# Optimization experiments

Hardware: AMD Instinct MI355X
Metric: run time of the kernel (lower is better)

Reference implementation:

```python
import jax, jax.numpy as jnp
import numpy as np


def _temperature_scales():
    s = np.arange(8, -3, -0.25).astype(np.float32)  # 44 levels
    s[-1] = 0.0
    return jnp.asarray(s)


def _pdist2(x, y):
    # squared euclidean distance matrix: [B,N,M]
    x_norm = jnp.sum(x * x, axis=2, keepdims=True)          # [B,N,1]
    y_norm = jnp.sum(y * y, axis=2, keepdims=True)          # [B,M,1]
    cross = jnp.einsum('bnd,bmd->bnm', x, y)
    return x_norm - 2.0 * cross + jnp.swapaxes(y_norm, 1, 2)


def _compute_match(points_x, points_y):
    b, n, _ = points_x.shape
    _, m, _ = points_y.shape
    max_size = max(n, m)
    factorl = max_size / n
    factorr = max_size / m
    d2 = _pdist2(points_x, points_y)                        # [B,N,M]
    satl0 = jnp.full((b, n), factorl, dtype=points_x.dtype)
    satr0 = jnp.full((b, m), factorr, dtype=points_x.dtype)
    match0 = jnp.zeros_like(d2)

    def step(carry, level):
        satl, satr, match = carry
        log_sr = jnp.log(satr[:, None, :] + 1e-30)          # [B,1,M]
        weight = jax.nn.softmax(d2 * level + log_sr, axis=-1)
        weight = weight * satl[:, :, None]
        ss = jnp.sum(weight, axis=1, keepdims=True) + 1e-09  # [B,1,M]
        ss = jnp.minimum(satr[:, None, :] / ss, 1.0)
        weight = weight * ss
        s = jnp.sum(weight, axis=2)                          # [B,N]
        ss2 = jnp.sum(weight, axis=1)                        # [B,M]
        satl = jnp.maximum(satl - s, 0.0)
        satr = jnp.maximum(satr - ss2, 0.0)
        match = match + weight
        return (satl, satr, match), None

    (_, _, match), _ = jax.lax.scan(step, (satl0, satr0, match0), _temperature_scales())
    return jax.lax.stop_gradient(match)


def setup_inputs() -> dict:
    key = jax.random.key(0)
    kx, ky = jax.random.split(key)
    B, N, M, D = 16, 2048, 2048, 3
    return {
        'points_x': jax.random.normal(kx, (B, N, D), dtype=jnp.float32),
        'points_y': jax.random.normal(ky, (B, M, D), dtype=jnp.float32),
    }


def reference(points_x, points_y):
    match = _compute_match(points_x, points_y)               # [B,N,M], detached
    d2 = _pdist2(points_x, points_y)                         # [B,N,M]
    loss = jnp.mean(jnp.sum(match * d2, axis=(1, 2)))
    return loss
```

## Files before the change

### kernel.cpp

```cpp
#include <hip/hip_runtime.h>

constexpr int NB = 16, NN = 2048, NM = 2048;
constexpr float LOG2E = 1.4426950408889634f;

#define EXP2 __builtin_amdgcn_exp2f
#define LOG2 __builtin_amdgcn_logf

constexpr size_t W_SATL  = 0;
constexpr size_t W_SATR  = 32768;
constexpr size_t W_ROWA  = 65536;
constexpr size_t W_ROWB  = 65536 + 4*32768;
constexpr size_t W_SPART = W_ROWB + 4*32768;
constexpr size_t W_LOSS  = W_SPART + (size_t)NB*32*NN;

__global__ __launch_bounds__(256) void k_init(float* ws) {
  int i = blockIdx.x*256 + threadIdx.x;
  if (i < NB*NM) ws[W_SATR + i] = 1.0f;
  if (i == 0) ws[W_LOSS] = 0.0f;
}

__global__ __launch_bounds__(512) void k_rows(const float* __restrict__ px,
                                              const float* __restrict__ py,
                                              float* __restrict__ ws,
                                              float lvl2, int first) {
  __shared__ float4 cpk[NM];
  const int b  = blockIdx.x >> 5;
  const int rb = blockIdx.x & 31;
  const int tid = threadIdx.x;

  {
    const float* satr = ws + W_SATR + (size_t)b*NM;
    const float4* pyv = (const float4*)(py + (size_t)b*NM*3);
    float4 pA = pyv[tid*3+0], pB = pyv[tid*3+1], pC = pyv[tid*3+2];
    float yy[12] = {pA.x,pA.y,pA.z,pA.w, pB.x,pB.y,pB.z,pB.w, pC.x,pC.y,pC.z,pC.w};
    #pragma unroll
    for (int k = 0; k < 4; ++k) {
      int col = tid*4 + k;
      float y0 = yy[3*k], y1 = yy[3*k+1], y2 = yy[3*k+2];
      float yn = y0*y0 + y1*y1 + y2*y2;
      float c  = fmaf(yn, lvl2, LOG2(satr[col] + 1e-30f));
      cpk[col] = make_float4(y0, y1, y2, c);
    }
  }
  __syncthreads();

  const int rloc = tid >> 3;
  const int q    = tid & 7;
  const int row  = rb*64 + rloc;
  const size_t gn = (size_t)b*NN + row;
  float x0 = px[gn*3+0], x1 = px[gn*3+1], x2 = px[gn*3+2];
  float xn = x0*x0 + x1*x1 + x2*x2;
  float an = xn * lvl2;
  float scl = -2.0f * lvl2;
  float xs0 = scl*x0, xs1 = scl*x1, xs2 = scl*x2;

  float rmax = -3.402823466e38f, rsum = 0.0f;
  for (int c8 = 0; c8 < 32; ++c8) {
    float l[8];
    #pragma unroll
    for (int i = 0; i < 8; ++i) {
      int col = (c8*8 + i)*8 + q;
      float4 p = cpk[col];
      l[i] = fmaf(xs0, p.x, fmaf(xs1, p.y, fmaf(xs2, p.z, p.w + an)));
    }
    float m01 = fmaxf(l[0], l[1]), m23 = fmaxf(l[2], l[3]);
    float m45 = fmaxf(l[4], l[5]), m67 = fmaxf(l[6], l[7]);
    float cm  = fmaxf(fmaxf(m01, m23), fmaxf(m45, m67));
    float nm  = fmaxf(rmax, cm);
    float cs = 0.0f;
    #pragma unroll
    for (int i = 0; i < 8; ++i) cs += EXP2(l[i] - nm);
    rsum = fmaf(rsum, EXP2(rmax - nm), cs);
    rmax = nm;
  }

  float sp = 0.0f;
  if (!first) {
    const float* spart = ws + W_SPART + ((size_t)b*32)*NN;
    #pragma unroll
    for (int i = 0; i < 4; ++i) sp += spart[(size_t)(q*4 + i)*NN + row];
  }

  #pragma unroll
  for (int d = 1; d <= 4; d <<= 1) {
    float om  = __shfl_xor(rmax, d);
    float od  = __shfl_xor(rsum, d);
    float osp = __shfl_xor(sp,  d);
    float nm  = fmaxf(rmax, om);
    rsum = rsum*EXP2(rmax - nm) + od*EXP2(om - nm);
    rmax = nm;
    sp += osp;
  }

  if (q == 0) {
    float sl = first ? 1.0f : ws[W_SATL + gn];
    sl = fmaxf(sl - sp, 0.0f);
    ws[W_SATL + gn] = sl;
    float rs2 = LOG2(sl / rsum) - rmax;
    float4* rowA = (float4*)(ws + W_ROWA);
    float4* rowB = (float4*)(ws + W_ROWB);
    rowA[gn] = make_float4(xs0, xs1, xs2, rs2 + an);
    rowB[gn] = make_float4(x0, x1, x2, rs2);
  }
}

__global__ __launch_bounds__(512) void k_cols(const float* __restrict__ py,
                                              float* __restrict__ ws,
                                              float lvl2) {
  __shared__ float4 rowLDS[NN];
  __shared__ float  sspart[8][64];
  __shared__ float4 colLDS[64];
  __shared__ float  lred[8];
  const int tid = threadIdx.x;
  const int wv = tid >> 6, lane = tid & 63;
  const int b = blockIdx.x >> 5, tile = blockIdx.x & 31;
  const int col = tile*64 + lane;
  const size_t gm = (size_t)b*NM + col;

  float y0 = py[gm*3+0], y1 = py[gm*3+1], y2 = py[gm*3+2];
  float yn = y0*y0 + y1*y1 + y2*y2;
  float sr  = ws[W_SATR + gm];
  float lsr = LOG2(sr + 1e-30f);
  float cB  = fmaf(yn, lvl2, lsr);

  const float4* gRowA = (const float4*)(ws + W_ROWA) + (size_t)b*NN;
  for (int i = tid; i < NN; i += 512) rowLDS[i] = gRowA[i];
  __syncthreads();

  const int n0 = wv * 256;
  float acc = 0.0f;
  #pragma unroll 8
  for (int n = n0; n < n0 + 256; ++n) {
    float4 r = rowLDS[n];
    float t = fmaf(r.x, y0, fmaf(r.y, y1, fmaf(r.z, y2, r.w + cB)));
    acc += EXP2(t);
  }
  sspart[wv][lane] = acc;
  __syncthreads();
  if (wv == 0) {
    float S = 0.0f;
    #pragma unroll
    for (int w = 0; w < 8; ++w) S += sspart[w][lane];
    float ssc = fminf(sr / (S + 1e-9f), 1.0f);
    float cC  = lsr + LOG2(ssc);
    ws[W_SATR + gm] = fmaxf(sr - S*ssc, 0.0f);
    colLDS[lane] = make_float4(y0, y1, y2, cC);
  }
  __syncthreads();

  const float4* gRowB = (const float4*)(ws + W_ROWB) + (size_t)b*NN;
  float* spart = ws + W_SPART + ((size_t)b*32 + tile)*NN;
  float4 r0 = gRowB[0*512 + tid];
  float4 r1 = gRowB[1*512 + tid];
  float4 r2 = gRowB[2*512 + tid];
  float4 r3 = gRowB[3*512 + tid];
  float s0 = 0.f, s1 = 0.f, s2 = 0.f, s3 = 0.f;
  float lossa = 0.0f;
  #pragma unroll 4
  for (int c = 0; c < 64; ++c) {
    float4 cv = colLDS[c];
    {
      float d0 = r0.x-cv.x, d1 = r0.y-cv.y, dz = r0.z-cv.z;
      float d2 = fmaf(d0,d0, fmaf(d1,d1, dz*dz));
      float w  = EXP2(fmaf(d2, lvl2, r0.w + cv.w));
      lossa = fmaf(w, d2, lossa); s0 += w;
    }
    {
      float d0 = r1.x-cv.x, d1 = r1.y-cv.y, dz = r1.z-cv.z;
      float d2 = fmaf(d0,d0, fmaf(d1,d1, dz*dz));
      float w  = EXP2(fmaf(d2, lvl2, r1.w + cv.w));
      lossa = fmaf(w, d2, lossa); s1 += w;
    }
    {
      float d0 = r2.x-cv.x, d1 = r2.y-cv.y, dz = r2.z-cv.z;
      float d2 = fmaf(d0,d0, fmaf(d1,d1, dz*dz));
      float w  = EXP2(fmaf(d2, lvl2, r2.w + cv.w));
      lossa = fmaf(w, d2, lossa); s2 += w;
    }
    {
      float d0 = r3.x-cv.x, d1 = r3.y-cv.y, dz = r3.z-cv.z;
      float d2 = fmaf(d0,d0, fmaf(d1,d1, dz*dz));
      float w  = EXP2(fmaf(d2, lvl2, r3.w + cv.w));
      lossa = fmaf(w, d2, lossa); s3 += w;
    }
  }
  spart[0*512 + tid] = s0;
  spart[1*512 + tid] = s1;
  spart[2*512 + tid] = s2;
  spart[3*512 + tid] = s3;

  #pragma unroll
  for (int d = 32; d >= 1; d >>= 1) lossa += __shfl_xor(lossa, d);
  if (lane == 0) lred[wv] = lossa;
  __syncthreads();
  if (tid == 0) {
    float t = 0.f;
    #pragma unroll
    for (int w = 0; w < 8; ++w) t += lred[w];
    atomicAdd(ws + W_LOSS, t);
  }
}

__global__ void k_final(const float* __restrict__ ws, float* __restrict__ out) {
  out[0] = ws[W_LOSS] * (1.0f / (float)NB);
}

extern "C" void kernel_launch(void* const* d_in, const int* in_sizes, int n_in,
                              void* d_out, int out_size, void* d_ws, size_t ws_size,
                              hipStream_t stream) {
  const float* px = (const float*)d_in[0];
  const float* py = (const float*)d_in[1];
  float* ws  = (float*)d_ws;
  float* out = (float*)d_out;

  k_init<<<dim3((NB*NM + 255)/256), dim3(256), 0, stream>>>(ws);
  for (int lv = 0; lv < 44; ++lv) {
    float level = (lv == 43) ? 0.0f : (8.0f - 0.25f*(float)lv);
    float lvl2 = level * LOG2E;
    k_rows<<<dim3(NB*32), dim3(512), 0, stream>>>(px, py, ws, lvl2, lv == 0 ? 1 : 0);
    k_cols<<<dim3(NB*32), dim3(512), 0, stream>>>(py, ws, lvl2);
  }
  k_final<<<dim3(1), dim3(1), 0, stream>>>(ws, out);
}
```

Before: 2.542 ms.

## Interleave row/column pairs and use packed FP32 FMA math

Row and column data move from one float4 per point to a pair-interleaved layout (x of two points, y of two points, and so on), so the distance and logit arithmetic can run as two-wide packed FP32 FMA, max and add ops. This applies to the softmax pass in the row kernel and to both passes in the column kernel. The row-kernel writeback becomes scattered scalar stores to match the new layout. The aim is to cut VALU instruction count, while exp2 stays scalar, and the changed LDS and global access pattern may alter bank conflicts or store efficiency.

```diff
diff --git a/kernel.cpp b/kernel.cpp
--- a/kernel.cpp
+++ b/kernel.cpp
@@ -5,6 +5,16 @@
 
 #define EXP2 __builtin_amdgcn_exp2f
 #define LOG2 __builtin_amdgcn_logf
+
+typedef float f32x2 __attribute__((ext_vector_type(2)));
+typedef float f32x4 __attribute__((ext_vector_type(4)));
+
+static __device__ __forceinline__ f32x2 pk_fma(f32x2 a, f32x2 b, f32x2 c) {
+  return __builtin_elementwise_fma(a, b, c);
+}
+static __device__ __forceinline__ f32x2 pk_max(f32x2 a, f32x2 b) {
+  return __builtin_elementwise_max(a, b);
+}
 
 constexpr size_t W_SATL  = 0;
 constexpr size_t W_SATR  = 32768;
@@ -23,7 +33,7 @@
                                               const float* __restrict__ py,
                                               float* __restrict__ ws,
                                               float lvl2, int first) {
-  __shared__ float4 cpk[NM];
+  __shared__ f32x4 cpk[NM];
   const int b  = blockIdx.x >> 5;
   const int rb = blockIdx.x & 31;
   const int tid = threadIdx.x;
@@ -33,13 +43,21 @@
     const float4* pyv = (const float4*)(py + (size_t)b*NM*3);
     float4 pA = pyv[tid*3+0], pB = pyv[tid*3+1], pC = pyv[tid*3+2];
     float yy[12] = {pA.x,pA.y,pA.z,pA.w, pB.x,pB.y,pB.z,pB.w, pC.x,pC.y,pC.z,pC.w};
+    float cm[4];
     #pragma unroll
     for (int k = 0; k < 4; ++k) {
       int col = tid*4 + k;
       float y0 = yy[3*k], y1 = yy[3*k+1], y2 = yy[3*k+2];
       float yn = y0*y0 + y1*y1 + y2*y2;
-      float c  = fmaf(yn, lvl2, LOG2(satr[col] + 1e-30f));
-      cpk[col] = make_float4(y0, y1, y2, c);
+      cm[k] = fmaf(yn, lvl2, LOG2(satr[col] + 1e-30f));
+    }
+    #pragma unroll
+    for (int k2 = 0; k2 < 2; ++k2) {
+      int ka = 2*k2, kb = 2*k2+1;
+      f32x4 lo = {yy[3*ka], yy[3*kb], yy[3*ka+1], yy[3*kb+1]};
+      f32x4 hi = {yy[3*ka+2], yy[3*kb+2], cm[ka], cm[kb]};
+      cpk[(2*tid + k2)*2 + 0] = lo;
+      cpk[(2*tid + k2)*2 + 1] = hi;
     }
   }
   __syncthreads();
@@ -53,23 +71,25 @@
   float an = xn * lvl2;
   float scl = -2.0f * lvl2;
   float xs0 = scl*x0, xs1 = scl*x1, xs2 = scl*x2;
+  f32x2 xs0p = {xs0,xs0}, xs1p = {xs1,xs1}, xs2p = {xs2,xs2}, anp = {an,an};
 
   float rmax = -3.402823466e38f, rsum = 0.0f;
   for (int c8 = 0; c8 < 32; ++c8) {
-    float l[8];
-    #pragma unroll
-    for (int i = 0; i < 8; ++i) {
-      int col = (c8*8 + i)*8 + q;
-      float4 p = cpk[col];
-      l[i] = fmaf(xs0, p.x, fmaf(xs1, p.y, fmaf(xs2, p.z, p.w + an)));
-    }
-    float m01 = fmaxf(l[0], l[1]), m23 = fmaxf(l[2], l[3]);
-    float m45 = fmaxf(l[4], l[5]), m67 = fmaxf(l[6], l[7]);
-    float cm  = fmaxf(fmaxf(m01, m23), fmaxf(m45, m67));
+    f32x2 lp[4];
+    #pragma unroll
+    for (int i = 0; i < 4; ++i) {
+      int pj = (c8*4 + i)*8 + q;
+      f32x4 a  = cpk[2*pj];
+      f32x4 b2 = cpk[2*pj+1];
+      lp[i] = pk_fma(xs0p, a.xy, pk_fma(xs1p, a.zw, pk_fma(xs2p, b2.xy, b2.zw + anp)));
+    }
+    f32x2 mp = pk_max(pk_max(lp[0], lp[1]), pk_max(lp[2], lp[3]));
+    float cm  = fmaxf(mp.x, mp.y);
     float nm  = fmaxf(rmax, cm);
-    float cs = 0.0f;
-    #pragma unroll
-    for (int i = 0; i < 8; ++i) cs += EXP2(l[i] - nm);
+    f32x2 nms = {nm, nm};
+    f32x2 e0 = lp[0] - nms, e1 = lp[1] - nms, e2 = lp[2] - nms, e3 = lp[3] - nms;
+    float cs = ((EXP2(e0.x) + EXP2(e0.y)) + (EXP2(e1.x) + EXP2(e1.y)))
+             + ((EXP2(e2.x) + EXP2(e2.y)) + (EXP2(e3.x) + EXP2(e3.y)));
     rsum = fmaf(rsum, EXP2(rmax - nm), cs);
     rmax = nm;
   }
@@ -97,17 +117,18 @@
     sl = fmaxf(sl - sp, 0.0f);
     ws[W_SATL + gn] = sl;
     float rs2 = LOG2(sl / rsum) - rmax;
-    float4* rowA = (float4*)(ws + W_ROWA);
-    float4* rowB = (float4*)(ws + W_ROWB);
-    rowA[gn] = make_float4(xs0, xs1, xs2, rs2 + an);
-    rowB[gn] = make_float4(x0, x1, x2, rs2);
+    size_t pbase = (size_t)b*NN*4 + (size_t)(row >> 1)*8 + (row & 1);
+    float* A  = ws + W_ROWA + pbase;
+    float* Bq = ws + W_ROWB + pbase;
+    A[0] = xs0; A[2] = xs1; A[4] = xs2; A[6] = rs2 + an;
+    Bq[0] = x0; Bq[2] = x1; Bq[4] = x2; Bq[6] = rs2;
   }
 }
 
 __global__ __launch_bounds__(512) void k_cols(const float* __restrict__ py,
                                               float* __restrict__ ws,
                                               float lvl2) {
-  __shared__ float4 rowLDS[NN];
+  __shared__ f32x4 rowLDS[NN];
   __shared__ float  sspart[8][64];
   __shared__ float4 colLDS[64];
   __shared__ float  lred[8];
@@ -123,19 +144,22 @@
   float lsr = LOG2(sr + 1e-30f);
   float cB  = fmaf(yn, lvl2, lsr);
 
-  const float4* gRowA = (const float4*)(ws + W_ROWA) + (size_t)b*NN;
+  const f32x4* gRowA = (const f32x4*)(ws + W_ROWA) + (size_t)b*NN;
   for (int i = tid; i < NN; i += 512) rowLDS[i] = gRowA[i];
   __syncthreads();
 
-  const int n0 = wv * 256;
-  float acc = 0.0f;
+  const int p0 = wv * 128;
+  f32x2 y0p = {y0,y0}, y1p = {y1,y1}, y2p = {y2,y2}, cBp = {cB,cB};
+  f32x2 accp = {0.f, 0.f};
   #pragma unroll 8
-  for (int n = n0; n < n0 + 256; ++n) {
-    float4 r = rowLDS[n];
-    float t = fmaf(r.x, y0, fmaf(r.y, y1, fmaf(r.z, y2, r.w + cB)));
-    acc += EXP2(t);
-  }
-  sspart[wv][lane] = acc;
+  for (int j = p0; j < p0 + 128; ++j) {
+    f32x4 a  = rowLDS[2*j];
+    f32x4 b2 = rowLDS[2*j+1];
+    f32x2 t = pk_fma(a.xy, y0p, pk_fma(a.zw, y1p, pk_fma(b2.xy, y2p, b2.zw + cBp)));
+    accp.x += EXP2(t.x);
+    accp.y += EXP2(t.y);
+  }
+  sspart[wv][lane] = accp.x + accp.y;
   __syncthreads();
   if (wv == 0) {
     float S = 0.0f;
@@ -148,47 +172,35 @@
   }
   __syncthreads();
 
-  const float4* gRowB = (const float4*)(ws + W_ROWB) + (size_t)b*NN;
+  const f32x4* gRowB = (const f32x4*)(ws + W_ROWB) + (size_t)b*NN;
   float* spart = ws + W_SPART + ((size_t)b*32 + tile)*NN;
-  float4 r0 = gRowB[0*512 + tid];
-  float4 r1 = gRowB[1*512 + tid];
-  float4 r2 = gRowB[2*512 + tid];
-  float4 r3 = gRowB[3*512 + tid];
-  float s0 = 0.f, s1 = 0.f, s2 = 0.f, s3 = 0.f;
-  float lossa = 0.0f;
+  f32x4 p0a = gRowB[2*tid],        p0b = gRowB[2*tid+1];
+  f32x4 p1a = gRowB[2*(tid+512)],  p1b = gRowB[2*(tid+512)+1];
+  f32x2 sA = {0,0}, sB = {0,0}, lossp = {0,0};
+  f32x2 L2p = {lvl2, lvl2};
   #pragma unroll 4
   for (int c = 0; c < 64; ++c) {
     float4 cv = colLDS[c];
+    f32x2 cx = {cv.x,cv.x}, cy = {cv.y,cv.y}, cz = {cv.z,cv.z}, cw = {cv.w,cv.w};
     {
-      float d0 = r0.x-cv.x, d1 = r0.y-cv.y, dz = r0.z-cv.z;
-      float d2 = fmaf(d0,d0, fmaf(d1,d1, dz*dz));
-      float w  = EXP2(fmaf(d2, lvl2, r0.w + cv.w));
-      lossa = fmaf(w, d2, lossa); s0 += w;
+      f32x2 d0 = p0a.xy - cx, d1 = p0a.zw - cy, dz = p0b.xy - cz;
+      f32x2 d2 = pk_fma(d0, d0, pk_fma(d1, d1, dz*dz));
+      f32x2 tt = pk_fma(d2, L2p, p0b.zw + cw);
+      f32x2 w; w.x = EXP2(tt.x); w.y = EXP2(tt.y);
+      lossp = pk_fma(w, d2, lossp); sA += w;
     }
     {
-      float d0 = r1.x-cv.x, d1 = r1.y-cv.y, dz = r1.z-cv.z;
-      float d2 = fmaf(d0,d0, fmaf(d1,d1, dz*dz));
-      float w  = EXP2(fmaf(d2, lvl2, r1.w + cv.w));
-      lossa = fmaf(w, d2, lossa); s1 += w;
-    }
-    {
-      float d0 = r2.x-cv.x, d1 = r2.y-cv.y, dz = r2.z-cv.z;
-      float d2 = fmaf(d0,d0, fmaf(d1,d1, dz*dz));
-      float w  = EXP2(fmaf(d2, lvl2, r2.w + cv.w));
-      lossa = fmaf(w, d2, lossa); s2 += w;
-    }
-    {
-      float d0 = r3.x-cv.x, d1 = r3.y-cv.y, dz = r3.z-cv.z;
-      float d2 = fmaf(d0,d0, fmaf(d1,d1, dz*dz));
-      float w  = EXP2(fmaf(d2, lvl2, r3.w + cv.w));
-      lossa = fmaf(w, d2, lossa); s3 += w;
-    }
-  }
-  spart[0*512 + tid] = s0;
-  spart[1*512 + tid] = s1;
-  spart[2*512 + tid] = s2;
-  spart[3*512 + tid] = s3;
-
+      f32x2 d0 = p1a.xy - cx, d1 = p1a.zw - cy, dz = p1b.xy - cz;
+      f32x2 d2 = pk_fma(d0, d0, pk_fma(d1, d1, dz*dz));
+      f32x2 tt = pk_fma(d2, L2p, p1b.zw + cw);
+      f32x2 w; w.x = EXP2(tt.x); w.y = EXP2(tt.y);
+      lossp = pk_fma(w, d2, lossp); sB += w;
+    }
+  }
+  ((float2*)spart)[tid]       = make_float2(sA.x, sA.y);
+  ((float2*)spart)[tid + 512] = make_float2(sB.x, sB.y);
+
+  float lossa = lossp.x + lossp.y;
   #pragma unroll
   for (int d = 32; d >= 1; d >>= 1) lossa += __shfl_xor(lossa, d);
   if (lane == 0) lred[wv] = lossa;
```

Result: faster. 2.157 ms (-15.2%).
